# Optimization experiments

Hardware: AMD Instinct MI355X
Metric: run time of the kernel (lower is better)

Reference implementation:

```python
import jax, jax.numpy as jnp
import numpy as np

B, S, L, C, H, W_IMG = 4, 2, 1024, 128, 256, 256
HEADS1, D1 = 4, C // 4          # layer 1: 4 heads x 32 dims, concat
HEADS2, D2 = 1, C               # layer 2: 1 head x 128 dims, mean
LN_EPS = 1e-5
NEG_SLOPE = 0.2


def _xavier(k, shape):
    limit = float(np.sqrt(6.0 / (shape[0] + shape[1])))
    return jax.random.uniform(k, shape, jnp.float32, -limit, limit)


def setup_inputs() -> dict:
    key = jax.random.key(0)
    ks = jax.random.split(key, 10)
    seg_feats = jax.random.normal(ks[0], (B, S, L, C), jnp.float32)
    # integer segment labels in 0..L (0 = background), stored per forward spec
    seg_images = jax.random.randint(ks[1], (B, S, H, W_IMG), 0, L + 1, jnp.int32)
    seg_nums = jnp.full((B, S), L, jnp.int32)
    return {
        "seg_feats": seg_feats,
        "seg_images": seg_images,
        "seg_nums": seg_nums,
        "W1": _xavier(ks[2], (HEADS1 * D1, C)),   # Linear weight (out, in)
        "a_src1": _xavier(ks[3], (HEADS1, D1)),
        "a_dst1": _xavier(ks[4], (HEADS1, D1)),
        "W2": _xavier(ks[5], (HEADS2 * D2, C)),
        "a_src2": _xavier(ks[6], (HEADS2, D2)),
        "a_dst2": _xavier(ks[7], (HEADS2, D2)),
        "ln_gamma": jnp.ones((C,), jnp.float32),
        "ln_beta": jnp.zeros((C,), jnp.float32),
    }


def build_adjacency(seg):
    """seg: (H, W) int labels in 1..L (0 = background) -> (L, L) float adj with self-loops."""
    adj = jnp.eye(L, dtype=jnp.float32)

    def add_edges(adj, a, b):
        valid = (a > 0) & (b > 0) & (a != b)
        ai = jnp.clip(a - 1, 0, L - 1)
        bi = jnp.clip(b - 1, 0, L - 1)
        v = valid.astype(jnp.float32)
        adj = adj.at[ai, bi].max(v)
        return adj.at[bi, ai].max(v)

    pairs = [
        (seg[:, :-1], seg[:, 1:]),       # horizontal
        (seg[:-1, :], seg[1:, :]),       # vertical
        (seg[:-1, :-1], seg[1:, 1:]),    # diagonal \
        (seg[:-1, 1:], seg[1:, :-1]),    # diagonal /
    ]
    for a, b in pairs:
        adj = add_edges(adj, a.reshape(-1), b.reshape(-1))
    return adj


def _leaky_relu(x):
    return jnp.where(x >= 0, x, NEG_SLOPE * x)


def gat_layer(x, adj, W, a_src, a_dst, heads, d, concat):
    N = x.shape[0]
    Wf = (x @ W.T).reshape(N, heads, d)                     # (N, h, d)
    e_src = jnp.einsum('nhd,hd->nh', Wf, a_src)             # (N, h)
    e_dst = jnp.einsum('nhd,hd->nh', Wf, a_dst)             # (N, h)
    e = _leaky_relu(e_src[:, None, :] + e_dst[None, :, :])  # (N, N, h)
    e = jnp.where((adj == 0)[:, :, None], -jnp.inf, e)
    alpha = jax.nn.softmax(e, axis=1)                       # softmax over neighbours j
    h = jnp.einsum('ijh,jhd->ihd', alpha, Wf)               # (N, h, d)
    if concat:
        return jax.nn.elu(h.reshape(N, heads * d))
    return h.mean(axis=1)


def reference(seg_feats, seg_images, seg_nums, W1, a_src1, a_dst1,
              W2, a_src2, a_dst2, ln_gamma, ln_beta):
    feats = seg_feats.reshape(B * S, L, C)
    adjs = jax.vmap(build_adjacency)(seg_images.reshape(B * S, H, W_IMG))

    def enrich(f, adj):
        h = gat_layer(f, adj, W1, a_src1, a_dst1, HEADS1, D1, True)
        h = gat_layer(h, adj, W2, a_src2, a_dst2, HEADS2, D2, False)
        y = f + h
        mu = jnp.mean(y, axis=-1, keepdims=True)
        var = jnp.var(y, axis=-1, keepdims=True)
        return (y - mu) * jax.lax.rsqrt(var + LN_EPS) * ln_gamma + ln_beta

    out = jax.vmap(enrich)(feats, adjs)
    return out.reshape(B, S, L, C)
```

## Files before the change

### kernel.cpp

```cpp
#include <hip/hip_runtime.h>
#include <hip/hip_bf16.h>
#include <stdint.h>

#define LL 1024
#define CC 128
#define NG 8
#define NN (NG*LL)
typedef __hip_bfloat16 bf16;
typedef __attribute__((ext_vector_type(8))) short short8;
typedef __attribute__((ext_vector_type(4))) short short4v;
typedef __attribute__((ext_vector_type(4))) float f32x4;

__device__ __forceinline__ bool is_bf16_wire(const void* gamma) {
  return *(const uint32_t*)gamma == 0x3F803F80u;
}
__device__ __forceinline__ float ldw(const void* p, size_t i, bool bf) {
  return bf ? __bfloat162float(((const bf16*)p)[i]) : ((const float*)p)[i];
}
__device__ __forceinline__ uint32_t encf(float f) {
  uint32_t b = __float_as_uint(f);
  return (b & 0x80000000u) ? ~b : (b | 0x80000000u);
}
__device__ __forceinline__ float decf(uint32_t u) {
  return (u & 0x80000000u) ? __uint_as_float(u & 0x7FFFFFFFu) : __uint_as_float(~u);
}
__device__ __forceinline__ short f2bs(float x) {
  uint32_t u = __float_as_uint(x);
  u += 0x7FFFu + ((u >> 16) & 1u);
  return (short)(u >> 16);
}
__device__ __forceinline__ void cvt8(const void* src, bf16* dst, int i8, bool bf) {
  if (bf) {
    ((uint4*)dst)[i8] = ((const uint4*)src)[i8];
  } else {
    const float4* f = (const float4*)src;
    float4 a = f[2 * i8], b = f[2 * i8 + 1];
    short8 pk;
    pk[0] = f2bs(a.x); pk[1] = f2bs(a.y); pk[2] = f2bs(a.z); pk[3] = f2bs(a.w);
    pk[4] = f2bs(b.x); pk[5] = f2bs(b.y); pk[6] = f2bs(b.z); pk[7] = f2bs(b.w);
    *(short8*)&((short*)dst)[i8 * 8] = pk;
  }
}


__global__ __launch_bounds__(256) void k_front(
    const void* __restrict__ feats, const void* __restrict__ W1,
    const void* __restrict__ W2, const void* __restrict__ as1,
    const void* __restrict__ ad1, const void* __restrict__ as2,
    const void* __restrict__ ad2, const void* __restrict__ gamma,
    bf16* __restrict__ xb, bf16* __restrict__ Wb1, bf16* __restrict__ Wb2,
    bf16* __restrict__ sm, const int* __restrict__ img,
    uint8_t* __restrict__ adj) {
  int bid = blockIdx.x;
  if (bid < 512) {
    const bool bf = is_bf16_wire(gamma);
    int t = bid * 256 + threadIdx.x;
    cvt8(feats, xb, t, bf);
    if (t < 2048) {
      cvt8(W1, Wb1, t, bf);
    } else if (t < 4096) {
      cvt8(W2, Wb2, t - 2048, bf);
    } else if (t < 4160) {
      int j = t - 4096;
      const void* srcs[4] = {as1, ad1, as2, ad2};
      cvt8(srcs[j >> 4], sm + (j >> 4) * 128, j & 15, bf);
    }
  } else {
    int idx = (bid - 512) * 256 + threadIdx.x;
    int g = idx >> 16, p = idx & 65535;
    int y = p >> 8, x = p & 255;
    const int* im = img + g * 65536;
    uint8_t* A = adj + (size_t)g * (LL * LL);
    int a = im[p];
    if (a > 0) {
      int nxs[4] = {x + 1, x, x + 1, x - 1};
      int nys[4] = {y, y + 1, y + 1, y + 1};
#pragma unroll
      for (int d = 0; d < 4; d++) {
        int nx = nxs[d], ny = nys[d];
        if (nx < 0 || nx > 255 || ny > 255) continue;
        int b = im[ny * 256 + nx];
        if (b > 0 && b != a) {
          A[(size_t)(a - 1) * LL + (b - 1)] = 1;
          A[(size_t)(b - 1) * LL + (a - 1)] = 1;
        }
      }
    }
  }
}

template <int NH>
__device__ __forceinline__ void gemm_core(const short8 af[4],
    const bf16* __restrict__ Wb, const bf16* __restrict__ asb,
    const bf16* __restrict__ adb, bf16* __restrict__ WfT,
    float* __restrict__ es, float* __restrict__ ed,
    uint32_t* __restrict__ edmax, int n0, int lane) {
  int quad = lane >> 4, c = lane & 15;
  int g = n0 >> 10;
  f32x4 acc[8];
#pragma unroll
  for (int dt = 0; dt < 8; dt++) acc[dt] = (f32x4){0.f, 0.f, 0.f, 0.f};
#pragma unroll
  for (int ks = 0; ks < 4; ks++)
#pragma unroll
    for (int dt = 0; dt < 8; dt++) {
      short8 bfr = *(const short8*)&Wb[(size_t)(dt * 16 + c) * CC + ks * 32 + quad * 8];
      acc[dt] = __builtin_amdgcn_mfma_f32_16x16x32_bf16(af[ks], bfr, acc[dt], 0, 0, 0);
    }
  {
    int nw4 = ((n0 & 1023) >> 2) + quad;
    bf16* wdst = WfT + (size_t)g * 131072 + (size_t)nw4 * 512 + c * 4;
#pragma unroll
    for (int dt = 0; dt < 8; dt++) {
      short4v pk;
#pragma unroll
      for (int r = 0; r < 4; r++) pk[r] = f2bs(acc[dt][r]);
      *(short4v*)&wdst[dt * 64] = pk;
    }
  }
  float sv[NH][4], dv[NH][4];
#pragma unroll
  for (int h = 0; h < NH; h++)
#pragma unroll
    for (int r = 0; r < 4; r++) { sv[h][r] = 0.f; dv[h][r] = 0.f; }
#pragma unroll
  for (int dt = 0; dt < 8; dt++) {
    int o = dt * 16 + c;
    float a_s = __bfloat162float(asb[o]);
    float a_d = __bfloat162float(adb[o]);
    int h = (NH == 4) ? (dt >> 1) : 0;
#pragma unroll
    for (int r = 0; r < 4; r++) {
      sv[h][r] += acc[dt][r] * a_s;
      dv[h][r] += acc[dt][r] * a_d;
    }
  }
#pragma unroll
  for (int m = 1; m <= 8; m <<= 1)
#pragma unroll
    for (int h = 0; h < NH; h++)
#pragma unroll
      for (int r = 0; r < 4; r++) {
        sv[h][r] += __shfl_xor(sv[h][r], m);
        dv[h][r] += __shfl_xor(dv[h][r], m);
      }
  if (c == 0) {
#pragma unroll
    for (int r = 0; r < 4; r++) {
      int node = n0 + quad * 4 + r;
#pragma unroll
      for (int h = 0; h < NH; h++) {
        es[node * NH + h] = sv[h][r];
        ed[node * NH + h] = dv[h][r];
      }
    }
  }
  float mq[NH];
#pragma unroll
  for (int h = 0; h < NH; h++) {
    mq[h] = fmaxf(fmaxf(dv[h][0], dv[h][1]), fmaxf(dv[h][2], dv[h][3]));
    mq[h] = fmaxf(mq[h], __shfl_xor(mq[h], 16));
    mq[h] = fmaxf(mq[h], __shfl_xor(mq[h], 32));
  }
  if (lane == 0)
#pragma unroll
    for (int h = 0; h < NH; h++)
      atomicMax(&edmax[g * NH + h], encf(mq[h]));
}

__global__ __launch_bounds__(256) void k_mid(
    const uint8_t* __restrict__ adj, uint32_t* __restrict__ bits,
    const bf16* __restrict__ xb, const bf16* __restrict__ Wb1,
    const bf16* __restrict__ sm, bf16* __restrict__ WfT,
    float* __restrict__ es, float* __restrict__ ed,
    uint32_t* __restrict__ edmax) {
  int bid = blockIdx.x, t = threadIdx.x;
  if (bid < 1024) {
    int id = bid * 256 + t;
    const uint32_t* src = (const uint32_t*)(adj + (size_t)id * 32);
    uint32_t w = 0;
#pragma unroll
    for (int d = 0; d < 8; d++) {
      uint32_t v = src[d];
      uint32_t nib = (((v & 0x01010101u) * 0x01020408u) >> 24) & 0xFu;
      w |= nib << (4 * d);
    }
    int i = (id >> 5) & 1023, wd = id & 31;
    if ((i >> 5) == wd) w |= 1u << (i & 31);
    bits[id] = w;
  } else {
    int lane = t & 63, w = t >> 6;
    int quad = lane >> 4, c = lane & 15;
    int n0 = (bid - 1024) * 64 + w * 16;
    short8 af[4];
#pragma unroll
    for (int ks = 0; ks < 4; ks++)
      af[ks] = *(const short8*)&xb[(size_t)(n0 + c) * CC + ks * 32 + quad * 8];
    gemm_core<4>(af, Wb1, sm, sm + 128, WfT, es, ed, edmax, n0, lane);
  }
}

template <int NH>
__global__ __launch_bounds__(256) void k_attn(
    const bf16* __restrict__ WfT, const float* __restrict__ esb,
    const float* __restrict__ edb, const uint32_t* __restrict__ bits,
    const uint32_t* __restrict__ edmax, bf16* __restrict__ pacc,
    float* __restrict__ pml) {
  __shared__ __align__(16) float red[4224];
  __shared__ float eds[NH * 520];
  __shared__ float lred[4][16 * NH];
  int t = threadIdx.x;
  int lane = t & 63, w = t >> 6;
  int quad = lane >> 4, c = lane & 15;
  int bid = blockIdx.x;
  int jp = bid & 1, rt = (bid >> 1) & 63, g = bid >> 7;
  int i0 = rt * 16;
  int node = g * LL + i0 + c;
  int J0 = jp * 512 + w * 128;
  for (int u = t; u < 512 * NH; u += 256) {
    int h = u >> 9, j = u & 511;
    eds[h * 520 + j] = edb[(size_t)(g * LL + jp * 512 + j) * NH + h];
  }
  const float LOG2E = 1.44269504f;
  float esv[NH], cmv[NH];
  if (NH == 4) {
    const float4 e4 = *(const float4*)&esb[(size_t)node * 4];
    esv[0] = e4.x; esv[1] = e4.y; esv[2] = e4.z; esv[3] = e4.w;
  } else {
    esv[0] = esb[node];
  }
#pragma unroll
  for (int h = 0; h < NH; h++) {
    float mx = decf(edmax[NH == 4 ? g * 4 + h : g]);
    float m = esv[h] + mx; m = fmaxf(m, 0.2f * m);
    cmv[h] = -m * LOG2E;
  }
  uint4 mk = *(const uint4*)&bits[(size_t)node * 32 + jp * 16 + w * 4];
  const uint32_t mkw[4] = {mk.x, mk.y, mk.z, mk.w};
  f32x4 acc[8];
#pragma unroll
  for (int dt = 0; dt < 8; dt++) acc[dt] = (f32x4){0.f, 0.f, 0.f, 0.f};
  float lsum[NH];
#pragma unroll
  for (int h = 0; h < NH; h++) lsum[h] = 0.f;
  const bf16* wb = WfT + (size_t)g * 131072 + (size_t)J0 * 128 + quad * 1024 + c * 4;
  __syncthreads();

  union FB { uint2 u[2]; short8 s; };
#pragma unroll
  for (int jb = 0; jb < 4; jb++) {
    short8 frag[8];
#pragma unroll
    for (int dt = 0; dt < 8; dt++) {
      FB f;
      f.u[0] = *(const uint2*)&wb[jb * 4096 + dt * 64];
      f.u[1] = *(const uint2*)&wb[jb * 4096 + dt * 64 + 512];
      frag[dt] = f.s;
    }
    int base_wj = w * 128 + jb * 32 + quad * 8;
    uint32_t mw = mkw[jb] >> (quad * 8);
    float mf[8];
#pragma unroll
    for (int i = 0; i < 8; i++) mf[i] = (float)((mw >> i) & 1u);
#pragma unroll
    for (int h = 0; h < NH; h++) {
      const float* ep = &eds[h * 520 + base_wj];
      float4 ea = *(const float4*)ep;
      float4 eb = *(const float4*)(ep + 4);
      float ev[8] = {ea.x, ea.y, ea.z, ea.w, eb.x, eb.y, eb.z, eb.w};
      float pr[8];
      float lac = 0.f;
#pragma unroll
      for (int i = 0; i < 8; i++) {
        float e = esv[h] + ev[i];
        e = fmaxf(e, 0.2f * e);
        float p = exp2f(fmaf(e, LOG2E, cmv[h]));
        p *= mf[i];
        lac += p;
        pr[i] = p;
      }
      lsum[h] += lac;
      union { short8 s; uint32_t u[4]; } A;
#pragma unroll
      for (int k = 0; k < 4; k++) {
        __hip_bfloat162 q = __float22bfloat162_rn(make_float2(pr[2*k], pr[2*k+1]));
        A.u[k] = *reinterpret_cast<uint32_t*>(&q);
      }
#pragma unroll
      for (int d2 = 0; d2 < 8 / NH; d2++) {
        int dt = h * (8 / NH) + d2;
        acc[dt] = __builtin_amdgcn_mfma_f32_16x16x32_bf16(A.s, frag[dt], acc[dt], 0, 0, 0);
      }
    }
  }
#pragma unroll
  for (int h = 0; h < NH; h++) {
    float v = lsum[h];
    v += __shfl_xor(v, 16);
    v += __shfl_xor(v, 32);
    lsum[h] = v;
  }
  if (quad == 0)
#pragma unroll
    for (int h = 0; h < NH; h++) lred[w][c * NH + h] = lsum[h];
  if (w == 1)
#pragma unroll
    for (int dt = 0; dt < 8; dt++) *(f32x4*)&red[dt * 256 + lane * 4] = acc[dt];
  if (w == 3)
#pragma unroll
    for (int dt = 0; dt < 8; dt++) *(f32x4*)&red[2048 + dt * 256 + lane * 4] = acc[dt];
  __syncthreads();
  if (w == 0)
#pragma unroll
    for (int dt = 0; dt < 8; dt++) acc[dt] += *(const f32x4*)&red[dt * 256 + lane * 4];
  if (w == 2)
#pragma unroll
    for (int dt = 0; dt < 8; dt++) acc[dt] += *(const f32x4*)&red[2048 + dt * 256 + lane * 4];
  __syncthreads();
  if (w == 2)
#pragma unroll
    for (int dt = 0; dt < 8; dt++) *(f32x4*)&red[dt * 256 + lane * 4] = acc[dt];
  __syncthreads();
  if (w == 0) {
#pragma unroll
    for (int dt = 0; dt < 8; dt++) acc[dt] += *(const f32x4*)&red[dt * 256 + lane * 4];
#pragma unroll
    for (int dt = 0; dt < 8; dt++)
#pragma unroll
      for (int r = 0; r < 4; r++)
        red[2048 + (quad * 4 + r) * 132 + dt * 16 + c] = acc[dt][r];
  }
  __syncthreads();
  {
    int row = t >> 4, d0 = (t & 15) * 8;
    const float* src = &red[2048 + row * 132 + d0];
    short8 pk;
#pragma unroll
    for (int k = 0; k < 8; k++) pk[k] = f2bs(src[k]);
    *(short8*)&pacc[((size_t)jp * NN + g * LL + i0 + row) * CC + d0] = pk;
  }
  if (t < 16 * NH) {
    float l = lred[0][t] + lred[1][t] + lred[2][t] + lred[3][t];
    int row = (NH == 4) ? (t >> 2) : t;
    int h = (NH == 4) ? (t & 3) : 0;
    if (NH == 4) pml[((size_t)jp * NN + g * LL + i0 + row) * 4 + h] = l;
    else         pml[(size_t)jp * NN + g * LL + i0 + row] = l;
  }
}

__global__ __launch_bounds__(256) void k_gemm2c(
    const bf16* __restrict__ pacc, const float* __restrict__ pml1,
    const bf16* __restrict__ Wb2, const bf16* __restrict__ sm2,
    bf16* __restrict__ WfT, float* __restrict__ es, float* __restrict__ ed,
    uint32_t* __restrict__ edmax) {
  int t = threadIdx.x;
  int lane = t & 63, w = t >> 6;
  int quad = lane >> 4, c = lane & 15;
  int n0 = blockIdx.x * 64 + w * 16;
  int node = n0 + c;
  float4 l4 = make_float4(0.f, 0.f, 0.f, 0.f);
#pragma unroll
  for (int p = 0; p < 2; p++) {
    float4 v = *(const float4*)&pml1[((size_t)p * NN + node) * 4];
    l4.x += v.x; l4.y += v.y; l4.z += v.z; l4.w += v.w;
  }
  float linv[4] = {1.f / l4.x, 1.f / l4.y, 1.f / l4.z, 1.f / l4.w};
  short8 af[4];
#pragma unroll
  for (int ks = 0; ks < 4; ks++) {
    float a[8] = {0.f, 0.f, 0.f, 0.f, 0.f, 0.f, 0.f, 0.f};
#pragma unroll
    for (int p = 0; p < 2; p++) {
      short8 v = *(const short8*)&pacc[((size_t)p * NN + node) * CC + ks * 32 + quad * 8];
#pragma unroll
      for (int i = 0; i < 8; i++) {
        union { short s[2]; float f; } cv; cv.s[0] = 0; cv.s[1] = v[i];
        a[i] += cv.f;
      }
    }
#pragma unroll
    for (int i = 0; i < 8; i++) {
      float vv = a[i] * linv[ks];
      vv = (vv > 0.f) ? vv : (__expf(vv) - 1.f);
      af[ks][i] = f2bs(vv);
    }
  }
  gemm_core<1>(af, Wb2, sm2, sm2 + 128, WfT, es, ed, edmax, n0, lane);
}

__global__ __launch_bounds__(256) void k_combine2(const bf16* __restrict__ pacc,
    const float* __restrict__ pml2, const void* __restrict__ feats,
    const void* __restrict__ gamma, const void* __restrict__ beta,
    void* __restrict__ outp) {
  const bool bf = is_bf16_wire(gamma);
  int t = threadIdx.x;
  int node = blockIdx.x * 4 + (t >> 6);
  int lane = t & 63;
  float l = 0.f, a0 = 0.f, a1 = 0.f;
#pragma unroll
  for (int p = 0; p < 2; p++) {
    l  += pml2[(size_t)p * NN + node];
    a0 += __bfloat162float(pacc[((size_t)p * NN + node) * CC + lane]);
    a1 += __bfloat162float(pacc[((size_t)p * NN + node) * CC + 64 + lane]);
  }
  float y0 = ldw(feats, (size_t)node * CC + lane, bf) + a0 / l;
  float y1 = ldw(feats, (size_t)node * CC + 64 + lane, bf) + a1 / l;
  float s = y0 + y1, s2 = y0 * y0 + y1 * y1;
#pragma unroll
  for (int mm = 32; mm >= 1; mm >>= 1) { s += __shfl_xor(s, mm); s2 += __shfl_xor(s2, mm); }
  float mu = s * (1.f / 128.f);
  float var = fmaxf(s2 * (1.f / 128.f) - mu * mu, 0.f);
  float rs = rsqrtf(var + 1e-5f);
  float o0 = (y0 - mu) * rs * ldw(gamma, lane, bf) + ldw(beta, lane, bf);
  float o1 = (y1 - mu) * rs * ldw(gamma, 64 + lane, bf) + ldw(beta, 64 + lane, bf);
  if (bf) {
    ((bf16*)outp)[(size_t)node * CC + lane]      = __float2bfloat16(o0);
    ((bf16*)outp)[(size_t)node * CC + 64 + lane] = __float2bfloat16(o1);
  } else {
    ((float*)outp)[(size_t)node * CC + lane]      = o0;
    ((float*)outp)[(size_t)node * CC + 64 + lane] = o1;
  }
}

extern "C" void kernel_launch(void* const* d_in, const int* in_sizes, int n_in,
                              void* d_out, int out_size, void* d_ws, size_t ws_size,
                              hipStream_t stream) {
  const void* feats = d_in[0];
  const int*  imgs  = (const int*)d_in[1];
  const void* W1    = d_in[3];
  const void* as1   = d_in[4];
  const void* ad1   = d_in[5];
  const void* W2    = d_in[6];
  const void* as2   = d_in[7];
  const void* ad2   = d_in[8];
  const void* gamma = d_in[9];
  const void* beta  = d_in[10];

  char* ws = (char*)d_ws;
  uint8_t*  adj    = (uint8_t*)ws;
  uint32_t* edmax1 = (uint32_t*)(ws + 8388608);
  uint32_t* edmax2 = (uint32_t*)(ws + 8389632);
  uint32_t* bits   = (uint32_t*)(ws + 9437184);
  bf16*     xb     = (bf16*)(ws + 10485760);
  bf16*     Wb1    = (bf16*)(ws + 12582912);
  bf16*     Wb2    = (bf16*)(ws + 12615680);
  bf16*     sm     = (bf16*)(ws + 12648448);
  bf16*     WfT    = (bf16*)(ws + 12652544);
  float*    es1    = (float*)(ws + 16846848);
  float*    ed1    = (float*)(ws + 16977920);
  float*    es2    = (float*)(ws + 17108992);
  float*    ed2    = (float*)(ws + 17141760);
  float*    pml    = (float*)(ws + 17174528);
  bf16*     pacc   = (bf16*)(ws + 18223104);

  hipMemsetAsync(ws, 0, 8390656, stream);
  hipLaunchKernelGGL(k_front, dim3(2560), dim3(256), 0, stream,
                     feats, W1, W2, as1, ad1, as2, ad2, gamma,
                     xb, Wb1, Wb2, sm, imgs, adj);
  hipLaunchKernelGGL(k_mid, dim3(1152), dim3(256), 0, stream,
                     adj, bits, xb, Wb1, sm, WfT, es1, ed1, edmax1);
  hipLaunchKernelGGL((k_attn<4>), dim3(1024), dim3(256), 0, stream,
                     WfT, es1, ed1, bits, edmax1, pacc, pml);
  hipLaunchKernelGGL(k_gemm2c, dim3(128), dim3(256), 0, stream,
                     pacc, pml, Wb2, sm + 256, WfT, es2, ed2, edmax2);
  hipLaunchKernelGGL((k_attn<1>), dim3(1024), dim3(256), 0, stream,
                     WfT, es2, ed2, bits, edmax2, pacc, pml);
  hipLaunchKernelGGL(k_combine2, dim3(2048), dim3(256), 0, stream,
                     pacc, pml, feats, gamma, beta, d_out);
}
```

Before: 192.5 us.

## Build adjacency bitmask directly in LDS per row-slab, drop byte matrix pass

Adjacency construction now runs in 64 workgroups, one per 128-row slab of each graph. Each workgroup scans the whole image and sets bits with atomicOr into a 16 KB shared bitmask, then writes the packed bits straight to global memory. This removes the 8 MB byte-adjacency memset, the scattered byte stores and the separate byte-to-bit packing pass in the middle kernel, which becomes a plain GEMM kernel. The cost is that every image is scanned 8 times, each by only one workgroup of 256 threads, giving a long serial loop and low parallelism with possible LDS atomic contention.

After: 421.8 us. 119% more time.

```diff
diff --git a/kernel.cpp b/kernel.cpp
--- a/kernel.cpp
+++ b/kernel.cpp
@@ -50,7 +50,8 @@
     const void* __restrict__ ad2, const void* __restrict__ gamma,
     bf16* __restrict__ xb, bf16* __restrict__ Wb1, bf16* __restrict__ Wb2,
     bf16* __restrict__ sm, const int* __restrict__ img,
-    uint8_t* __restrict__ adj) {
+    uint32_t* __restrict__ bits) {
+  __shared__ uint32_t lb[4096];
   int bid = blockIdx.x;
   if (bid < 512) {
     const bool bf = is_bf16_wire(gamma);
@@ -66,25 +67,42 @@
       cvt8(srcs[j >> 4], sm + (j >> 4) * 128, j & 15, bf);
     }
   } else {
-    int idx = (bid - 512) * 256 + threadIdx.x;
-    int g = idx >> 16, p = idx & 65535;
-    int y = p >> 8, x = p & 255;
+    int wg = bid - 512;
+    int g = wg >> 3, r0 = (wg & 7) * 128;
+    int t = threadIdx.x;
+    for (int u = t; u < 4096; u += 256) lb[u] = 0;
+    __syncthreads();
     const int* im = img + g * 65536;
-    uint8_t* A = adj + (size_t)g * (LL * LL);
-    int a = im[p];
-    if (a > 0) {
-      int nxs[4] = {x + 1, x, x + 1, x - 1};
-      int nys[4] = {y, y + 1, y + 1, y + 1};
-#pragma unroll
-      for (int d = 0; d < 4; d++) {
-        int nx = nxs[d], ny = nys[d];
-        if (nx < 0 || nx > 255 || ny > 255) continue;
-        int b = im[ny * 256 + nx];
-        if (b > 0 && b != a) {
-          A[(size_t)(a - 1) * LL + (b - 1)] = 1;
-          A[(size_t)(b - 1) * LL + (a - 1)] = 1;
+    for (int k = 0; k < 256; k++) {
+      int p = k * 256 + t;
+      int y = p >> 8, x = p & 255;
+      int a = im[p];
+      if (a > 0) {
+        int nxs[4] = {x + 1, x, x + 1, x - 1};
+        int nys[4] = {y, y + 1, y + 1, y + 1};
+#pragma unroll
+        for (int d = 0; d < 4; d++) {
+          int nx = nxs[d], ny = nys[d];
+          if (nx < 0 || nx > 255 || ny > 255) continue;
+          int b = im[ny * 256 + nx];
+          if (b > 0 && b != a) {
+            int ra = a - 1, rb = b - 1;
+            if (ra >= r0 && ra < r0 + 128)
+              atomicOr(&lb[(ra - r0) * 32 + (rb >> 5)], 1u << (rb & 31));
+            if (rb >= r0 && rb < r0 + 128)
+              atomicOr(&lb[(rb - r0) * 32 + (ra >> 5)], 1u << (ra & 31));
+          }
         }
       }
+    }
+    __syncthreads();
+    uint32_t* dst = bits + g * 32768 + r0 * 32;
+    for (int u = t; u < 4096; u += 256) {
+      int r = u >> 5, wd = u & 31;
+      uint32_t v = lb[u];
+      int i = r0 + r;
+      if ((i >> 5) == wd) v |= 1u << (i & 31);
+      dst[u] = v;
     }
   }
 }
@@ -168,36 +186,20 @@
       atomicMax(&edmax[g * NH + h], encf(mq[h]));
 }
 
-__global__ __launch_bounds__(256) void k_mid(
-    const uint8_t* __restrict__ adj, uint32_t* __restrict__ bits,
+__global__ __launch_bounds__(256) void k_gemm1(
     const bf16* __restrict__ xb, const bf16* __restrict__ Wb1,
     const bf16* __restrict__ sm, bf16* __restrict__ WfT,
     float* __restrict__ es, float* __restrict__ ed,
     uint32_t* __restrict__ edmax) {
-  int bid = blockIdx.x, t = threadIdx.x;
-  if (bid < 1024) {
-    int id = bid * 256 + t;
-    const uint32_t* src = (const uint32_t*)(adj + (size_t)id * 32);
-    uint32_t w = 0;
-#pragma unroll
-    for (int d = 0; d < 8; d++) {
-      uint32_t v = src[d];
-      uint32_t nib = (((v & 0x01010101u) * 0x01020408u) >> 24) & 0xFu;
-      w |= nib << (4 * d);
-    }
-    int i = (id >> 5) & 1023, wd = id & 31;
-    if ((i >> 5) == wd) w |= 1u << (i & 31);
-    bits[id] = w;
-  } else {
-    int lane = t & 63, w = t >> 6;
-    int quad = lane >> 4, c = lane & 15;
-    int n0 = (bid - 1024) * 64 + w * 16;
-    short8 af[4];
-#pragma unroll
-    for (int ks = 0; ks < 4; ks++)
-      af[ks] = *(const short8*)&xb[(size_t)(n0 + c) * CC + ks * 32 + quad * 8];
-    gemm_core<4>(af, Wb1, sm, sm + 128, WfT, es, ed, edmax, n0, lane);
-  }
+  int t = threadIdx.x;
+  int lane = t & 63, w = t >> 6;
+  int quad = lane >> 4, c = lane & 15;
+  int n0 = blockIdx.x * 64 + w * 16;
+  short8 af[4];
+#pragma unroll
+  for (int ks = 0; ks < 4; ks++)
+    af[ks] = *(const short8*)&xb[(size_t)(n0 + c) * CC + ks * 32 + quad * 8];
+  gemm_core<4>(af, Wb1, sm, sm + 128, WfT, es, ed, edmax, n0, lane);
 }
 
 template <int NH>
@@ -437,9 +439,8 @@
   const void* beta  = d_in[10];
 
   char* ws = (char*)d_ws;
-  uint8_t*  adj    = (uint8_t*)ws;
-  uint32_t* edmax1 = (uint32_t*)(ws + 8388608);
-  uint32_t* edmax2 = (uint32_t*)(ws + 8389632);
+  uint32_t* edmax1 = (uint32_t*)(ws + 0);
+  uint32_t* edmax2 = (uint32_t*)(ws + 1024);
   uint32_t* bits   = (uint32_t*)(ws + 9437184);
   bf16*     xb     = (bf16*)(ws + 10485760);
   bf16*     Wb1    = (bf16*)(ws + 12582912);
@@ -453,12 +454,12 @@
   float*    pml    = (float*)(ws + 17174528);
   bf16*     pacc   = (bf16*)(ws + 18223104);
 
-  hipMemsetAsync(ws, 0, 8390656, stream);
-  hipLaunchKernelGGL(k_front, dim3(2560), dim3(256), 0, stream,
+  hipMemsetAsync(ws, 0, 2048, stream);
+  hipLaunchKernelGGL(k_front, dim3(576), dim3(256), 0, stream,
                      feats, W1, W2, as1, ad1, as2, ad2, gamma,
-                     xb, Wb1, Wb2, sm, imgs, adj);
-  hipLaunchKernelGGL(k_mid, dim3(1152), dim3(256), 0, stream,
-                     adj, bits, xb, Wb1, sm, WfT, es1, ed1, edmax1);
+                     xb, Wb1, Wb2, sm, imgs, bits);
+  hipLaunchKernelGGL(k_gemm1, dim3(128), dim3(256), 0, stream,
+                     xb, Wb1, sm, WfT, es1, ed1, edmax1);
   hipLaunchKernelGGL((k_attn<4>), dim3(1024), dim3(256), 0, stream,
                      WfT, es1, ed1, bits, edmax1, pacc, pml);
   hipLaunchKernelGGL(k_gemm2c, dim3(128), dim3(256), 0, stream,
```
